# Optimization experiments

Measured on AMD Instinct MI355X. Metric: run time of the kernel, lower is better.

## Reference

```python
import jax, jax.numpy as jnp
import numpy as np


def setup_inputs() -> dict:
    key = jax.random.key(0)
    k1, k2, k3, k4 = jax.random.split(key, 4)
    B, S, E, H = 8, 2048, 4096, 128  # batch, seq, embed, head_size
    scale = 1.0 / np.sqrt(E)
    return {
        "x": jax.random.normal(k1, (B, S, E), dtype=jnp.float32),
        "Wq": jax.random.normal(k2, (E, H), dtype=jnp.float32) * scale,
        "Wk": jax.random.normal(k3, (E, H), dtype=jnp.float32) * scale,
        "Wv": jax.random.normal(k4, (E, H), dtype=jnp.float32) * scale,
    }


def reference(x, Wq, Wk, Wv):
    # Single-head attention, non-flash branch, mask=None, eval-mode dropout.
    q = jnp.einsum("bse,eh->bsh", x, Wq)  # [B,S,H]
    k = jnp.einsum("bse,eh->bsh", x, Wk)
    v = jnp.einsum("bse,eh->bsh", x, Wv)
    head_size = k.shape[-1]
    scores = jnp.einsum("bqh,bkh->bqk", q, k) * (head_size ** -0.5)  # [B,S,S]
    attn = jax.nn.softmax(scores, axis=-1)
    out = jnp.einsum("bqk,bkh->bqh", attn, v)  # [B,S,H]
    return out
```

## Files before the change

### kernel.cpp

```cpp
#include <hip/hip_runtime.h>
#include <math.h>

typedef __bf16 bf16_t;
typedef bf16_t bf16x8 __attribute__((ext_vector_type(8)));
typedef float floatx4 __attribute__((ext_vector_type(4)));

#define MFMA(a, b, c) __builtin_amdgcn_mfma_f32_16x16x32_bf16(a, b, c, 0, 0, 0)

static constexpr int S = 2048, E = 4096, H = 128;

__device__ __forceinline__ void gl_lds16(const void* g, void* l) {
  __builtin_amdgcn_global_load_lds((const __attribute__((address_space(1))) void*)g,
                                   (__attribute__((address_space(3))) void*)l,
                                   16, 0, 0);
}

__global__ __launch_bounds__(256) void wt_kernel(const float* __restrict__ Wq,
                                                 const float* __restrict__ Wk,
                                                 const float* __restrict__ Wv,
                                                 bf16_t* __restrict__ Wt) {
  __shared__ bf16_t tile[64][130];
  int wb = blockIdx.x / 64;
  int eb = blockIdx.x % 64;
  const float* W = wb == 0 ? Wq : (wb == 1 ? Wk : Wv);
  int t = threadIdx.x;
  {
    int er = t >> 2, q = t & 3;
    const float4* src = (const float4*)(W + (size_t)(eb * 64 + er) * H + q * 32);
    for (int i = 0; i < 8; ++i) {
      float4 f = src[i];
      int c = q * 32 + i * 4;
      tile[er][c + 0] = (bf16_t)f.x; tile[er][c + 1] = (bf16_t)f.y;
      tile[er][c + 2] = (bf16_t)f.z; tile[er][c + 3] = (bf16_t)f.w;
    }
  }
  __syncthreads();
  {
    int h = t >> 1, half = t & 1;
    bf16_t buf[32];
    for (int j = 0; j < 32; ++j) buf[j] = tile[half * 32 + j][h];
    bf16_t* dst = Wt + (size_t)(wb * H + h) * E + eb * 64 + half * 32;
    for (int i = 0; i < 4; ++i) ((uint4*)dst)[i] = ((uint4*)buf)[i];
  }
}

__global__ __launch_bounds__(256, 3) void qkv_kernel(const float* __restrict__ X,
                                                     const bf16_t* __restrict__ Wt,
                                                     bf16_t* __restrict__ Qb,
                                                     bf16_t* __restrict__ Kb,
                                                     bf16_t* __restrict__ Vt) {
  __shared__ __align__(16) char smem[49152];

  int phys = blockIdx.x;
  int xcd = phys & 7, slot = phys >> 3;
  int trip = slot / 3, nb = slot % 3;
  int mBase = (xcd * 32 + trip) * 64;

  int t = threadIdx.x, lane = t & 63, w = t >> 6;
  int wr = w >> 1, wc = w & 1;
  int r16 = lane & 15, q4 = lane >> 4;

  floatx4 acc[2][4] = {};

  const float* xbase = X + (size_t)(mBase + (t >> 4)) * E + (t & 15) * 4;
  int wrow0 = lane >> 3, wg = lane & 7;

  float4 xa[4], xb[4];

#define FENCE() asm volatile("" ::: "memory")
#define WAITB(N)                                                                 \
  do {                                                                           \
    asm volatile("s_waitcnt vmcnt(" #N ") lgkmcnt(0)" ::: "memory");             \
    __builtin_amdgcn_s_barrier();                                                \
    asm volatile("" ::: "memory");                                               \
  } while (0)

#define LOAD_X(XR, K0)                                                           \
  _Pragma("unroll") for (int i = 0; i < 4; ++i)                                  \
      (XR)[i] = *(const float4*)(xbase + (size_t)(i * 16) * E + (K0));

#define STAGE_W(WOFF, K0)                                                        \
  _Pragma("unroll") for (int is = 0; is < 4; ++is) {                             \
    int row = w * 32 + is * 8 + wrow0;                                           \
    int g = wg ^ (row & 7);                                                      \
    gl_lds16(Wt + (size_t)(nb * 128 + row) * E + (K0) + g * 8,                   \
             smem + (WOFF) + (w * 32 + is * 8) * 128 + lane * 16);               \
  }

#define STAGE_X(XOFF, XR)                                                        \
  _Pragma("unroll") for (int i = 0; i < 4; ++i) {                                \
    int row = i * 16 + (t >> 4);                                                 \
    float4 f = (XR)[i];                                                          \
    bf16_t pk[4] = {(bf16_t)f.x, (bf16_t)f.y, (bf16_t)f.z, (bf16_t)f.w};         \
    int gg = ((t & 15) >> 1) ^ (row & 7);                                        \
    *(uint2*)(smem + (XOFF) + row * 128 + gg * 16 + (t & 1) * 8) = *(uint2*)pk;  \
  }

#define COMPUTE(XOFF, WOFF)                                                      \
  _Pragma("unroll") for (int kc = 0; kc < 2; ++kc) {                             \
    bf16x8 a[2], b[4];                                                           \
    _Pragma("unroll") for (int i = 0; i < 2; ++i) {                              \
      int row = wr * 32 + i * 16 + r16;                                          \
      int sl = (kc * 4 + q4) ^ (row & 7);                                        \
      a[i] = *(const bf16x8*)(smem + (XOFF) + row * 128 + sl * 16);              \
    }                                                                            \
    _Pragma("unroll") for (int j = 0; j < 4; ++j) {                              \
      int row = wc * 64 + j * 16 + r16;                                          \
      int sl = (kc * 4 + q4) ^ (row & 7);                                        \
      b[j] = *(const bf16x8*)(smem + (WOFF) + row * 128 + sl * 16);              \
    }                                                                            \
    _Pragma("unroll") for (int i = 0; i < 2; ++i)                                \
        _Pragma("unroll") for (int j = 0; j < 4; ++j)                            \
            acc[i][j] = MFMA(a[i], b[j], acc[i][j]);                             \
  }

  LOAD_X(xa, 0);
  FENCE();
  STAGE_W(8192, 0);
  STAGE_X(0, xa);
  FENCE();
  LOAD_X(xb, 64);
  WAITB(4);

  for (int kb = 0; kb < 64; kb += 2) {
    bool more = (kb < 62);
    STAGE_X(24576, xb);
    STAGE_W(32768, (kb + 1) * 64);
    FENCE();
    if (more) LOAD_X(xa, (kb + 2) * 64);
    COMPUTE(0, 8192);
    if (more) WAITB(4); else WAITB(0);

    if (more) {
      STAGE_X(0, xa);
      STAGE_W(8192, (kb + 2) * 64);
    }
    FENCE();
    if (more) LOAD_X(xb, (kb + 3) * 64);
    COMPUTE(24576, 32768);
    if (more) WAITB(4); else WAITB(0);
  }

  if (nb < 2) {
    bf16_t(*Ob)[136] = (bf16_t(*)[136])smem;
#pragma unroll
    for (int i = 0; i < 2; ++i)
#pragma unroll
      for (int j = 0; j < 4; ++j)
#pragma unroll
        for (int ii = 0; ii < 4; ++ii)
          Ob[wr * 32 + i * 16 + q4 * 4 + ii][wc * 64 + j * 16 + r16] =
              (bf16_t)acc[i][j][ii];
    __syncthreads();
    bf16_t* outp = (nb == 0 ? Qb : Kb) + (size_t)mBase * H;
    int row = t >> 2, cg = t & 3;
#pragma unroll
    for (int u = 0; u < 4; ++u)
      *(uint4*)(outp + (size_t)row * H + cg * 32 + u * 8) =
          *(uint4*)&Ob[row][cg * 32 + u * 8];
  } else {
    int bb = mBase >> 11;
    int sBase = mBase & 2047;
    bf16_t* vb = Vt + (size_t)bb * H * S;
#pragma unroll
    for (int i = 0; i < 2; ++i)
#pragma unroll
      for (int j = 0; j < 4; ++j) {
        int hcol = wc * 64 + j * 16 + r16;
        int srow = sBase + wr * 32 + i * 16 + q4 * 4;
        bf16_t pk[4];
#pragma unroll
        for (int ii = 0; ii < 4; ++ii) pk[ii] = (bf16_t)acc[i][j][ii];
        *(uint2*)&vb[(size_t)hcol * S + srow] = *(uint2*)pk;
      }
  }
#undef LOAD_X
#undef STAGE_W
#undef STAGE_X
#undef COMPUTE
#undef FENCE
#undef WAITB
}

__global__ __launch_bounds__(256, 2) void attn_kernel(const bf16_t* __restrict__ Qb,
                                                      const bf16_t* __restrict__ Kb,
                                                      const bf16_t* __restrict__ Vt,
                                                      float* __restrict__ Op,
                                                      float* __restrict__ Mp,
                                                      float* __restrict__ Lp) {
  __shared__ __align__(16) char smem[74752];

  int bid = blockIdx.x;
  int b = bid & 7, r = bid >> 3;
  int qt = r >> 1, half = r & 1;

  int t = threadIdx.x, lane = t & 63, wl = t >> 6;
  int r16 = lane & 15, q4 = lane >> 4;
  bf16_t(*Pl)[72] = (bf16_t(*)[72])(smem + 65536 + wl * 2304);

  bf16x8 qf[4];
  {
    const bf16_t* qp = Qb + (size_t)(b * S + qt * 64 + wl * 16 + r16) * H + q4 * 8;
#pragma unroll
    for (int c = 0; c < 4; ++c) qf[c] = *(const bf16x8*)(qp + c * 32);
  }
  floatx4 o[8] = {};
  float m_r[4], l_r[4];
#pragma unroll
  for (int ii = 0; ii < 4; ++ii) { m_r[ii] = -1e30f; l_r[ii] = 0.f; }
  const float scale = 0.08838834764831845f;

  int kr = lane >> 4, kg = lane & 15;
  int vr = lane >> 3, vg = lane & 7;

#define STAGE_KV(BUF, KT)                                                        \
  _Pragma("unroll") for (int is = 0; is < 4; ++is) {                             \
    int row = wl * 16 + is * 4 + kr;                                             \
    int g = kg ^ (row & 15);                                                     \
    gl_lds16(Kb + (size_t)(b * S + (KT) * 64 + row) * H + g * 8,                 \
             smem + (BUF) + (wl * 16 + is * 4) * 256 + lane * 16);               \
  }                                                                              \
  _Pragma("unroll") for (int is = 0; is < 4; ++is) {                             \
    int row = wl * 32 + is * 8 + vr;                                             \
    int g = vg ^ (row & 7);                                                      \
    gl_lds16(Vt + (size_t)(b * H + row) * S + (KT) * 64 + g * 8,                 \
             smem + (BUF) + 16384 + (wl * 32 + is * 8) * 128 + lane * 16);       \
  }

  STAGE_KV(0, half * 16);
  __syncthreads();

  for (int it = 0; it < 16; ++it) {
    int cur = (it & 1) << 15;
    if (it < 15) { STAGE_KV(cur ^ 32768, half * 16 + it + 1); }
    const char* kbase = smem + cur;
    bf16_t(*Vl)[64] = (bf16_t(*)[64])(smem + cur + 16384);

    floatx4 s4[4] = {};
#pragma unroll
    for (int c = 0; c < 4; ++c)
#pragma unroll
      for (int j = 0; j < 4; ++j) {
        int row = j * 16 + r16;
        int sl = (c * 4 + q4) ^ r16;
        bf16x8 bk = *(const bf16x8*)(kbase + row * 256 + sl * 16);
        s4[j] = MFMA(qf[c], bk, s4[j]);
      }

    float p[4][4], mx[4], ls[4], alpha[4];
#pragma unroll
    for (int ii = 0; ii < 4; ++ii) mx[ii] = -1e30f;
#pragma unroll
    for (int j = 0; j < 4; ++j)
#pragma unroll
      for (int ii = 0; ii < 4; ++ii) {
        float sv = s4[j][ii] * scale;
        p[j][ii] = sv;
        mx[ii] = fmaxf(mx[ii], sv);
      }
#pragma unroll
    for (int off = 1; off <= 8; off <<= 1)
#pragma unroll
      for (int ii = 0; ii < 4; ++ii)
        mx[ii] = fmaxf(mx[ii], __shfl_xor(mx[ii], off));
#pragma unroll
    for (int ii = 0; ii < 4; ++ii) {
      float mn = fmaxf(m_r[ii], mx[ii]);
      alpha[ii] = __expf(m_r[ii] - mn);
      m_r[ii] = mn;
      ls[ii] = 0.f;
    }
#pragma unroll
    for (int j = 0; j < 4; ++j)
#pragma unroll
      for (int ii = 0; ii < 4; ++ii) {
        float e = __expf(p[j][ii] - m_r[ii]);
        ls[ii] += e;
        Pl[q4 * 4 + ii][j * 16 + r16] = (bf16_t)e;
      }
#pragma unroll
    for (int off = 1; off <= 8; off <<= 1)
#pragma unroll
      for (int ii = 0; ii < 4; ++ii) ls[ii] += __shfl_xor(ls[ii], off);
#pragma unroll
    for (int ii = 0; ii < 4; ++ii) l_r[ii] = l_r[ii] * alpha[ii] + ls[ii];
#pragma unroll
    for (int f = 0; f < 8; ++f)
#pragma unroll
      for (int ii = 0; ii < 4; ++ii) o[f][ii] *= alpha[ii];

#pragma unroll
    for (int kc = 0; kc < 2; ++kc) {
      bf16x8 pa = *(const bf16x8*)&Pl[r16][kc * 32 + q4 * 8];
#pragma unroll
      for (int f = 0; f < 8; ++f) {
        int row = f * 16 + r16;
        int sl = (kc * 4 + q4) ^ (row & 7);
        bf16x8 bv = *(const bf16x8*)&Vl[row][sl * 8];
        o[f] = MFMA(pa, bv, o[f]);
      }
    }
    __syncthreads();
  }
#undef STAGE_KV

  int rowg = b * S + qt * 64 + wl * 16 + q4 * 4;
  float* op = Op + ((size_t)half * 16384 + rowg) * 128;
#pragma unroll
  for (int f = 0; f < 8; ++f)
#pragma unroll
    for (int ii = 0; ii < 4; ++ii)
      op[ii * 128 + f * 16 + r16] = o[f][ii];
  if (r16 == 0) {
#pragma unroll
    for (int ii = 0; ii < 4; ++ii) {
      Mp[half * 16384 + rowg + ii] = m_r[ii];
      Lp[half * 16384 + rowg + ii] = l_r[ii];
    }
  }
}

__global__ __launch_bounds__(256) void merge_kernel(const float* __restrict__ Op,
                                                    const float* __restrict__ Mp,
                                                    const float* __restrict__ Lp,
                                                    float* __restrict__ out) {
  int t = threadIdx.x;
  int row = blockIdx.x * 64 + (t >> 2);
  int c0 = (t & 3) * 32;
  float m1 = Mp[row], m2 = Mp[16384 + row];
  float l1 = Lp[row], l2 = Lp[16384 + row];
  float M = fmaxf(m1, m2);
  float e1 = __expf(m1 - M), e2 = __expf(m2 - M);
  float inv = 1.f / (e1 * l1 + e2 * l2);
  const float4* o1 = (const float4*)(Op + (size_t)row * 128 + c0);
  const float4* o2 = (const float4*)(Op + 16384ull * 128 + (size_t)row * 128 + c0);
  float4* op = (float4*)(out + (size_t)row * 128 + c0);
#pragma unroll
  for (int i = 0; i < 8; ++i) {
    float4 a = o1[i], b = o2[i];
    float4 rr;
    rr.x = (e1 * a.x + e2 * b.x) * inv;
    rr.y = (e1 * a.y + e2 * b.y) * inv;
    rr.z = (e1 * a.z + e2 * b.z) * inv;
    rr.w = (e1 * a.w + e2 * b.w) * inv;
    op[i] = rr;
  }
}

extern "C" void kernel_launch(void* const* d_in, const int* in_sizes, int n_in,
                              void* d_out, int out_size, void* d_ws, size_t ws_size,
                              hipStream_t stream) {
  const float* x = (const float*)d_in[0];
  const float* Wq = (const float*)d_in[1];
  const float* Wk = (const float*)d_in[2];
  const float* Wv = (const float*)d_in[3];
  float* out = (float*)d_out;

  bf16_t* Wt = (bf16_t*)d_ws;
  bf16_t* Qb = Wt + (size_t)384 * 4096;
  bf16_t* Kb = Qb + (size_t)16384 * 128;
  bf16_t* Vt = Kb + (size_t)16384 * 128;
  float* Op = (float*)(Vt + (size_t)8 * 128 * 2048);
  float* Mp = Op + (size_t)2 * 16384 * 128;
  float* Lp = Mp + 2 * 16384;

  wt_kernel<<<192, 256, 0, stream>>>(Wq, Wk, Wv, Wt);
  qkv_kernel<<<768, 256, 0, stream>>>(x, Wt, Qb, Kb, Vt);
  attn_kernel<<<512, 256, 0, stream>>>(Qb, Kb, Vt, Op, Mp, Lp);
  merge_kernel<<<256, 256, 0, stream>>>(Op, Mp, Lp, out);
}
```

Baseline: 468.1 us.

## Fuse Q/K/V projections into one 64x384 tile per block to read X once

The QKV projection previously launched three blocks per 64-row slice of x, one each for Q, K and V, so every x tile was loaded and converted three times. Now each 512-thread block computes all 384 output columns for its 64 rows, with 8 waves each owning 48 columns. That cuts global reads of the fp32 x, the dominant traffic, by about a factor of three. In exchange it uses about 112KB of LDS, limiting occupancy, launches only 256 blocks, and drops the XCD-aware block mapping.

New measurement: 459.3 us. About the same (-1.9%).

```diff
diff --git a/kernel.cpp b/kernel.cpp
--- a/kernel.cpp
+++ b/kernel.cpp
@@ -44,28 +44,25 @@
   }
 }
 
-__global__ __launch_bounds__(256, 3) void qkv_kernel(const float* __restrict__ X,
+__global__ __launch_bounds__(512, 2) void qkv_kernel(const float* __restrict__ X,
                                                      const bf16_t* __restrict__ Wt,
                                                      bf16_t* __restrict__ Qb,
                                                      bf16_t* __restrict__ Kb,
                                                      bf16_t* __restrict__ Vt) {
-  __shared__ __align__(16) char smem[49152];
-
-  int phys = blockIdx.x;
-  int xcd = phys & 7, slot = phys >> 3;
-  int trip = slot / 3, nb = slot % 3;
-  int mBase = (xcd * 32 + trip) * 64;
-
+  __shared__ __align__(16) char smem[114688];
+  constexpr int B0X = 0, B0W = 8192, B1X = 57344, B1W = 65536;
+
+  int mBase = blockIdx.x * 64;
   int t = threadIdx.x, lane = t & 63, w = t >> 6;
-  int wr = w >> 1, wc = w & 1;
   int r16 = lane & 15, q4 = lane >> 4;
 
-  floatx4 acc[2][4] = {};
-
-  const float* xbase = X + (size_t)(mBase + (t >> 4)) * E + (t & 15) * 4;
-  int wrow0 = lane >> 3, wg = lane & 7;
-
-  float4 xa[4], xb[4];
+  floatx4 acc[4][3] = {};
+
+  int xrow = t >> 3;
+  const float* xbase = X + (size_t)(mBase + xrow) * E + (t & 7) * 4;
+  int wrl = lane >> 3, wg = lane & 7;
+
+  float4 xa[2], xb[2];
 
 #define FENCE() asm volatile("" ::: "memory")
 #define WAITB(N)                                                                 \
@@ -76,103 +73,109 @@
   } while (0)
 
 #define LOAD_X(XR, K0)                                                           \
-  _Pragma("unroll") for (int i = 0; i < 4; ++i)                                  \
-      (XR)[i] = *(const float4*)(xbase + (size_t)(i * 16) * E + (K0));
+  _Pragma("unroll") for (int i = 0; i < 2; ++i)                                  \
+      (XR)[i] = *(const float4*)(xbase + (K0) + i * 32);
 
 #define STAGE_W(WOFF, K0)                                                        \
-  _Pragma("unroll") for (int is = 0; is < 4; ++is) {                             \
-    int row = w * 32 + is * 8 + wrow0;                                           \
+  _Pragma("unroll") for (int is = 0; is < 6; ++is) {                             \
+    int row = w * 48 + is * 8 + wrl;                                             \
     int g = wg ^ (row & 7);                                                      \
-    gl_lds16(Wt + (size_t)(nb * 128 + row) * E + (K0) + g * 8,                   \
-             smem + (WOFF) + (w * 32 + is * 8) * 128 + lane * 16);               \
+    gl_lds16(Wt + (size_t)row * E + (K0) + g * 8,                                \
+             smem + (WOFF) + (w * 48 + is * 8) * 128 + lane * 16);               \
   }
 
 #define STAGE_X(XOFF, XR)                                                        \
-  _Pragma("unroll") for (int i = 0; i < 4; ++i) {                                \
-    int row = i * 16 + (t >> 4);                                                 \
+  _Pragma("unroll") for (int i = 0; i < 2; ++i) {                                \
     float4 f = (XR)[i];                                                          \
     bf16_t pk[4] = {(bf16_t)f.x, (bf16_t)f.y, (bf16_t)f.z, (bf16_t)f.w};         \
-    int gg = ((t & 15) >> 1) ^ (row & 7);                                        \
-    *(uint2*)(smem + (XOFF) + row * 128 + gg * 16 + (t & 1) * 8) = *(uint2*)pk;  \
+    int gc = ((t & 7) >> 1) + i * 4;                                             \
+    int g = gc ^ (xrow & 7);                                                     \
+    *(uint2*)(smem + (XOFF) + xrow * 128 + g * 16 + (t & 1) * 8) = *(uint2*)pk;  \
   }
 
 #define COMPUTE(XOFF, WOFF)                                                      \
   _Pragma("unroll") for (int kc = 0; kc < 2; ++kc) {                             \
-    bf16x8 a[2], b[4];                                                           \
-    _Pragma("unroll") for (int i = 0; i < 2; ++i) {                              \
-      int row = wr * 32 + i * 16 + r16;                                          \
+    bf16x8 a[4], b[3];                                                           \
+    _Pragma("unroll") for (int i = 0; i < 4; ++i) {                              \
+      int row = i * 16 + r16;                                                    \
       int sl = (kc * 4 + q4) ^ (row & 7);                                        \
       a[i] = *(const bf16x8*)(smem + (XOFF) + row * 128 + sl * 16);              \
     }                                                                            \
-    _Pragma("unroll") for (int j = 0; j < 4; ++j) {                              \
-      int row = wc * 64 + j * 16 + r16;                                          \
+    _Pragma("unroll") for (int j = 0; j < 3; ++j) {                              \
+      int row = w * 48 + j * 16 + r16;                                           \
       int sl = (kc * 4 + q4) ^ (row & 7);                                        \
       b[j] = *(const bf16x8*)(smem + (WOFF) + row * 128 + sl * 16);              \
     }                                                                            \
-    _Pragma("unroll") for (int i = 0; i < 2; ++i)                                \
-        _Pragma("unroll") for (int j = 0; j < 4; ++j)                            \
+    _Pragma("unroll") for (int i = 0; i < 4; ++i)                                \
+        _Pragma("unroll") for (int j = 0; j < 3; ++j)                            \
             acc[i][j] = MFMA(a[i], b[j], acc[i][j]);                             \
   }
 
   LOAD_X(xa, 0);
   FENCE();
-  STAGE_W(8192, 0);
-  STAGE_X(0, xa);
+  STAGE_W(B0W, 0);
+  FENCE();
+  STAGE_X(B0X, xa);
   FENCE();
   LOAD_X(xb, 64);
-  WAITB(4);
-
-  for (int kb = 0; kb < 64; kb += 2) {
-    bool more = (kb < 62);
-    STAGE_X(24576, xb);
-    STAGE_W(32768, (kb + 1) * 64);
-    FENCE();
-    if (more) LOAD_X(xa, (kb + 2) * 64);
-    COMPUTE(0, 8192);
-    if (more) WAITB(4); else WAITB(0);
-
-    if (more) {
-      STAGE_X(0, xa);
-      STAGE_W(8192, (kb + 2) * 64);
-    }
-    FENCE();
-    if (more) LOAD_X(xb, (kb + 3) * 64);
-    COMPUTE(24576, 32768);
-    if (more) WAITB(4); else WAITB(0);
-  }
-
-  if (nb < 2) {
-    bf16_t(*Ob)[136] = (bf16_t(*)[136])smem;
-#pragma unroll
-    for (int i = 0; i < 2; ++i)
-#pragma unroll
-      for (int j = 0; j < 4; ++j)
+  WAITB(2);
+
+  for (int kb = 0; kb < 62; kb += 2) {
+    STAGE_W(B1W, (kb + 1) * 64);
+    FENCE();
+    STAGE_X(B1X, xb);
+    FENCE();
+    LOAD_X(xa, (kb + 2) * 64);
+    FENCE();
+    COMPUTE(B0X, B0W);
+    WAITB(2);
+
+    STAGE_W(B0W, (kb + 2) * 64);
+    FENCE();
+    STAGE_X(B0X, xa);
+    FENCE();
+    LOAD_X(xb, (kb + 3) * 64);
+    FENCE();
+    COMPUTE(B1X, B1W);
+    WAITB(2);
+  }
+  STAGE_W(B1W, 63 * 64);
+  FENCE();
+  STAGE_X(B1X, xb);
+  FENCE();
+  COMPUTE(B0X, B0W);
+  WAITB(0);
+  COMPUTE(B1X, B1W);
+
+  int bb = mBase >> 11, sBase = mBase & 2047;
+  bf16_t(*Ob)[264] = (bf16_t(*)[264])smem;
+#pragma unroll
+  for (int i = 0; i < 4; ++i)
+#pragma unroll
+    for (int j = 0; j < 3; ++j) {
+      int ncol = w * 48 + j * 16;
+      if (ncol >= 256) {
+        int h = ncol - 256 + r16;
+        bf16_t pk[4];
+#pragma unroll
+        for (int ii = 0; ii < 4; ++ii) pk[ii] = (bf16_t)acc[i][j][ii];
+        *(uint2*)&Vt[((size_t)bb * H + h) * S + sBase + i * 16 + q4 * 4] =
+            *(uint2*)pk;
+      } else {
 #pragma unroll
         for (int ii = 0; ii < 4; ++ii)
-          Ob[wr * 32 + i * 16 + q4 * 4 + ii][wc * 64 + j * 16 + r16] =
-              (bf16_t)acc[i][j][ii];
-    __syncthreads();
-    bf16_t* outp = (nb == 0 ? Qb : Kb) + (size_t)mBase * H;
-    int row = t >> 2, cg = t & 3;
-#pragma unroll
-    for (int u = 0; u < 4; ++u)
-      *(uint4*)(outp + (size_t)row * H + cg * 32 + u * 8) =
-          *(uint4*)&Ob[row][cg * 32 + u * 8];
-  } else {
-    int bb = mBase >> 11;
-    int sBase = mBase & 2047;
-    bf16_t* vb = Vt + (size_t)bb * H * S;
-#pragma unroll
-    for (int i = 0; i < 2; ++i)
-#pragma unroll
-      for (int j = 0; j < 4; ++j) {
-        int hcol = wc * 64 + j * 16 + r16;
-        int srow = sBase + wr * 32 + i * 16 + q4 * 4;
-        bf16_t pk[4];
-#pragma unroll
-        for (int ii = 0; ii < 4; ++ii) pk[ii] = (bf16_t)acc[i][j][ii];
-        *(uint2*)&vb[(size_t)hcol * S + srow] = *(uint2*)pk;
-      }
+          Ob[i * 16 + q4 * 4 + ii][ncol + r16] = (bf16_t)acc[i][j][ii];
+      }
+    }
+  __syncthreads();
+  {
+    int row = t >> 3, g = t & 7;
+    bf16_t* qp = Qb + (size_t)(mBase + row) * H + g * 16;
+    bf16_t* kp = Kb + (size_t)(mBase + row) * H + g * 16;
+    *(uint4*)qp = *(uint4*)&Ob[row][g * 16];
+    *(uint4*)(qp + 8) = *(uint4*)&Ob[row][g * 16 + 8];
+    *(uint4*)kp = *(uint4*)&Ob[row][128 + g * 16];
+    *(uint4*)(kp + 8) = *(uint4*)&Ob[row][128 + g * 16 + 8];
   }
 #undef LOAD_X
 #undef STAGE_W
@@ -365,7 +368,7 @@
   float* Lp = Mp + 2 * 16384;
 
   wt_kernel<<<192, 256, 0, stream>>>(Wq, Wk, Wv, Wt);
-  qkv_kernel<<<768, 256, 0, stream>>>(x, Wt, Qb, Kb, Vt);
+  qkv_kernel<<<256, 512, 0, stream>>>(x, Wt, Qb, Kb, Vt);
   attn_kernel<<<512, 256, 0, stream>>>(Qb, Kb, Vt, Op, Mp, Lp);
   merge_kernel<<<256, 256, 0, stream>>>(Op, Mp, Lp, out);
 }
```
